# Kernel optimization log

Hardware: AMD Instinct MI355X
Metric: run time of the kernel (lower is better)

## Reference

```python
import jax, jax.numpy as jnp
import numpy as np

D_MODEL = 1024
NUM_HEADS = 16
D_K = D_MODEL // NUM_HEADS
BATCH = 2
SEQ = 2048


def setup_inputs() -> dict:
    key = jax.random.key(0)
    ks = jax.random.split(key, 11)
    s = 1.0 / np.sqrt(D_MODEL)
    return {
        "query": jax.random.normal(ks[0], (BATCH, SEQ, D_MODEL), jnp.float32),
        "key_": jax.random.normal(ks[1], (BATCH, SEQ, D_MODEL), jnp.float32),
        "value": jax.random.normal(ks[2], (BATCH, SEQ, D_MODEL), jnp.float32),
        "w_q": jax.random.uniform(ks[3], (D_MODEL, D_MODEL), jnp.float32, -s, s),
        "b_q": jax.random.uniform(ks[4], (D_MODEL,), jnp.float32, -s, s),
        "w_k": jax.random.uniform(ks[5], (D_MODEL, D_MODEL), jnp.float32, -s, s),
        "b_k": jax.random.uniform(ks[6], (D_MODEL,), jnp.float32, -s, s),
        "w_v": jax.random.uniform(ks[7], (D_MODEL, D_MODEL), jnp.float32, -s, s),
        "b_v": jax.random.uniform(ks[8], (D_MODEL,), jnp.float32, -s, s),
        "w_o": jax.random.uniform(ks[9], (D_MODEL, D_MODEL), jnp.float32, -s, s),
        "b_o": jax.random.uniform(ks[10], (D_MODEL,), jnp.float32, -s, s),
    }


def reference(query, key_, value, w_q, b_q, w_k, b_k, w_v, b_v, w_o, b_o):
    B, S, D = query.shape
    H, dk = NUM_HEADS, D_K

    def proj(x, w, b):
        # torch Linear: x @ w.T + b ; reshape to (B, H, S, dk)
        return (x @ w.T + b).reshape(B, S, H, dk).transpose(0, 2, 1, 3)

    Q = proj(query, w_q, b_q)
    K = proj(key_, w_k, b_k)
    V = proj(value, w_v, b_v)

    scores = jnp.einsum("bhqd,bhkd->bhqk", Q, K) / jnp.sqrt(jnp.float32(dk))
    attn = jax.nn.softmax(scores, axis=-1)  # dropout is identity in eval
    ctx = jnp.einsum("bhqk,bhkd->bhqd", attn, V)
    ctx = ctx.transpose(0, 2, 1, 3).reshape(B, S, D)
    out = ctx @ w_o.T + b_o
    return out
```

## Files before the change

### kernel.cpp

```cpp
#include <hip/hip_runtime.h>
#include <cstdint>
#include <cstddef>

typedef unsigned short u16;
typedef short bf16x8 __attribute__((ext_vector_type(8)));
typedef unsigned short u16x8 __attribute__((ext_vector_type(8)));
typedef float f32x4 __attribute__((ext_vector_type(4)));

#define NHEAD 16
#define SEQ 2048
#define DMODEL 1024
#define BATCH 2
#define QSCALE 0.18033688011112042f

__device__ __forceinline__ float exp2_fast(float x) {
  return __builtin_amdgcn_exp2f(x);
}

__device__ __forceinline__ u16 f2bf(float f) {
  union { float f; unsigned u; } v; v.f = f;
  return (u16)((v.u + 0x7fffu + ((v.u >> 16) & 1u)) >> 16);
}

__device__ __forceinline__ int swz(int row, int colbyte) {
  return (row << 7) + (colbyte ^ ((row & 7) << 4));
}

__device__ __forceinline__ void load_lds16(const void* g, void* lds) {
  __builtin_amdgcn_global_load_lds(
      (const __attribute__((address_space(1))) unsigned int*)g,
      (__attribute__((address_space(3))) unsigned int*)lds, 16, 0, 0);
}

__global__ __launch_bounds__(256) void convall(
    const float* __restrict__ q, const float* __restrict__ k, const float* __restrict__ v,
    const float* __restrict__ wq, const float* __restrict__ wk,
    const float* __restrict__ wv, const float* __restrict__ wo,
    u16* __restrict__ Xq, u16* __restrict__ Xk, u16* __restrict__ Xv,
    u16* __restrict__ Wq, u16* __restrict__ Wk, u16* __restrict__ Wv,
    u16* __restrict__ Wo) {
  int bid = blockIdx.x;
  const float* in;
  u16* out;
  int local;
  if (bid < 6144) {
    int a = bid >> 11;
    local = bid & 2047;
    in = a == 0 ? q : a == 1 ? k : v;
    out = a == 0 ? Xq : a == 1 ? Xk : Xv;
  } else {
    int bb = bid - 6144;
    int a = bb >> 9;
    local = bb & 511;
    in = a == 0 ? wq : a == 1 ? wk : a == 2 ? wv : wo;
    out = a == 0 ? Wq : a == 1 ? Wk : a == 2 ? Wv : Wo;
  }
  int i = local * 256 + threadIdx.x;
  const float4* p = (const float4*)in + (size_t)i * 2;
  float4 a4 = p[0], b4 = p[1];
  u16x8 o;
  o[0] = f2bf(a4.x); o[1] = f2bf(a4.y); o[2] = f2bf(a4.z); o[3] = f2bf(a4.w);
  o[4] = f2bf(b4.x); o[5] = f2bf(b4.y); o[6] = f2bf(b4.z); o[7] = f2bf(b4.w);
  *((u16x8*)out + i) = o;
}

__global__ __launch_bounds__(256) void gemm_qkv(
    const u16* __restrict__ A0, const u16* __restrict__ A1, const u16* __restrict__ A2,
    const u16* __restrict__ W0, const u16* __restrict__ W1, const u16* __restrict__ W2,
    const float* __restrict__ b0, const float* __restrict__ b1, const float* __restrict__ b2,
    u16* __restrict__ C0, u16* __restrict__ C1, u16* __restrict__ C2) {
  constexpr int K = 1024;
  __shared__ u16 Ash[128 * 32];
  __shared__ u16 Bsh[128 * 32];
  const int z = blockIdx.z;
  const u16* A = z == 0 ? A0 : z == 1 ? A1 : A2;
  const u16* W = z == 0 ? W0 : z == 1 ? W1 : W2;
  const float* bias = z == 0 ? b0 : z == 1 ? b1 : b2;
  u16* C = z == 0 ? C0 : z == 1 ? C1 : C2;
  const float scale = z == 0 ? QSCALE : 1.0f;

  const int t = threadIdx.x;
  const int w = t >> 6;
  const int l = t & 63;
  const int m0 = (blockIdx.x * 4 + (blockIdx.y >> 3)) * 128;
  const int n0 = (blockIdx.y & 7) * 128;
  const int wm = (w >> 1) * 64;
  const int wn = (w & 1) * 64;
  const int lr = l & 15;
  const int hi = l >> 4;
  const int lk = hi * 8;
  const int srow = l >> 2;
  const int scol = (l & 3) * 8;

  f32x4 acc[4][4] = {};

  for (int k0 = 0; k0 < K; k0 += 32) {
#pragma unroll
    for (int c = 0; c < 2; ++c) {
      int ra = (c * 4 + w) * 16 + srow;
      load_lds16(A + (size_t)(m0 + ra) * K + k0 + scol, &Ash[(c * 4 + w) * 512]);
      load_lds16(W + (size_t)(n0 + ra) * K + k0 + scol, &Bsh[(c * 4 + w) * 512]);
    }
    __syncthreads();
    bf16x8 af[4], bfr[4];
#pragma unroll
    for (int i = 0; i < 4; ++i)
      af[i] = *(const bf16x8*)&Ash[(wm + i * 16 + lr) * 32 + lk];
#pragma unroll
    for (int j = 0; j < 4; ++j)
      bfr[j] = *(const bf16x8*)&Bsh[(wn + j * 16 + lr) * 32 + lk];
#pragma unroll
    for (int i = 0; i < 4; ++i)
#pragma unroll
      for (int j = 0; j < 4; ++j)
        acc[i][j] = __builtin_amdgcn_mfma_f32_16x16x32_bf16(af[i], bfr[j], acc[i][j], 0, 0, 0);
    __syncthreads();
  }

#pragma unroll
  for (int i = 0; i < 4; ++i)
#pragma unroll
    for (int j = 0; j < 4; ++j)
#pragma unroll
      for (int r = 0; r < 4; ++r) {
        int row = m0 + wm + i * 16 + hi * 4 + r;
        int col = n0 + wn + j * 16 + lr;
        float v = (acc[i][j][r] + bias[col]) * scale;
        int b = row >> 11, s = row & 2047;
        int h = col >> 6, d = col & 63;
        C[(((size_t)(b * NHEAD + h) * SEQ + s) << 6) + d] = f2bf(v);
      }
}

__global__ __launch_bounds__(256) void gemm_o(const u16* __restrict__ A,
                                              const u16* __restrict__ W,
                                              const float* __restrict__ bias,
                                              float* __restrict__ C) {
  constexpr int K = 1024;
  __shared__ u16 Ash[64 * 32];
  __shared__ u16 Bsh[128 * 32];
  const int t = threadIdx.x;
  const int w = t >> 6;
  const int l = t & 63;
  const int m0 = (blockIdx.x * 8 + (blockIdx.y >> 3)) * 64;
  const int n0 = (blockIdx.y & 7) * 128;
  const int wm = (w >> 1) * 32;
  const int wn = (w & 1) * 64;
  const int lr = l & 15;
  const int hi = l >> 4;
  const int lk = hi * 8;
  const int srow = l >> 2;
  const int scol = (l & 3) * 8;

  f32x4 acc[2][4] = {};

  for (int k0 = 0; k0 < K; k0 += 32) {
    {
      int ra = w * 16 + srow;
      load_lds16(A + (size_t)(m0 + ra) * K + k0 + scol, &Ash[w * 512]);
    }
#pragma unroll
    for (int c = 0; c < 2; ++c) {
      int rb = (c * 4 + w) * 16 + srow;
      load_lds16(W + (size_t)(n0 + rb) * K + k0 + scol, &Bsh[(c * 4 + w) * 512]);
    }
    __syncthreads();
    bf16x8 af[2], bfr[4];
#pragma unroll
    for (int i = 0; i < 2; ++i)
      af[i] = *(const bf16x8*)&Ash[(wm + i * 16 + lr) * 32 + lk];
#pragma unroll
    for (int j = 0; j < 4; ++j)
      bfr[j] = *(const bf16x8*)&Bsh[(wn + j * 16 + lr) * 32 + lk];
#pragma unroll
    for (int i = 0; i < 2; ++i)
#pragma unroll
      for (int j = 0; j < 4; ++j)
        acc[i][j] = __builtin_amdgcn_mfma_f32_16x16x32_bf16(af[i], bfr[j], acc[i][j], 0, 0, 0);
    __syncthreads();
  }

#pragma unroll
  for (int i = 0; i < 2; ++i)
#pragma unroll
    for (int j = 0; j < 4; ++j)
#pragma unroll
      for (int r = 0; r < 4; ++r) {
        int row = m0 + wm + i * 16 + hi * 4 + r;
        int col = n0 + wn + j * 16 + lr;
        C[(size_t)row * DMODEL + col] = acc[i][j][r] + bias[col];
      }
}

__global__ __launch_bounds__(256) void transpose_v(const u16* __restrict__ V,
                                                   u16* __restrict__ Vt) {
  __shared__ u16 tile[64][72];
  int st = blockIdx.x, bh = blockIdx.y;
  int t = threadIdx.x;
  {
    int s = t >> 2, part = (t & 3) * 16;
    const u16* g = V + (((size_t)bh * SEQ + st * 64 + s) << 6) + part;
    u16x8 v0 = *(const u16x8*)&g[0];
    u16x8 v1 = *(const u16x8*)&g[8];
    *(u16x8*)&tile[s][part] = v0;
    *(u16x8*)&tile[s][part + 8] = v1;
  }
  __syncthreads();
  {
    int d = t >> 2, sp = (t & 3) * 16;
    u16x8 o0, o1;
#pragma unroll
    for (int j = 0; j < 8; ++j) {
      int c0 = sp + j, c1 = sp + 8 + j;
      o0[j] = tile[(c0 & 3) * 16 + (c0 >> 2)][d];
      o1[j] = tile[(c1 & 3) * 16 + (c1 >> 2)][d];
    }
    u16* out = Vt + ((size_t)bh * 64 + d) * SEQ + st * 64 + sp;
    *(u16x8*)&out[0] = o0;
    *(u16x8*)&out[8] = o1;
  }
}

__device__ __forceinline__ void attn_tile(
    int kt, bool pf, const u16* Kg, const u16* Vg, int srow, int scb,
    char* QsB, char* KsC, char* VsC, char* KsN, char* VsN,
    bf16x8 (&qf)[2][2], f32x4 (&acc)[2][4], float (&lsum)[2][4],
    int w, int lr, int hi) {
  u16x8 nk0, nk1, nv0, nv1;
  if (pf) {
    const u16* kg = Kg + (kt + 1) * 4096;
    const u16* vg = Vg + (kt + 1) * 64;
    nk0 = *(const u16x8*)&kg[srow * 64 + scb / 2];
    nk1 = *(const u16x8*)&kg[srow * 64 + scb / 2 + 8];
    nv0 = *(const u16x8*)&vg[(size_t)srow * SEQ + scb / 2];
    nv1 = *(const u16x8*)&vg[(size_t)srow * SEQ + scb / 2 + 8];
  }

  f32x4 sc[2][4] = {};
  __builtin_amdgcn_s_setprio(1);
#pragma unroll
  for (int ks = 0; ks < 2; ++ks) {
    bf16x8 kb[4];
#pragma unroll
    for (int nt = 0; nt < 4; ++nt)
      kb[nt] = *(const bf16x8*)(KsC + swz(nt * 16 + lr, ks * 64 + hi * 16));
#pragma unroll
    for (int mt = 0; mt < 2; ++mt)
#pragma unroll
      for (int nt = 0; nt < 4; ++nt)
        sc[mt][nt] = __builtin_amdgcn_mfma_f32_16x16x32_bf16(qf[mt][ks], kb[nt], sc[mt][nt], 0, 0, 0);
  }
  __builtin_amdgcn_s_setprio(0);

#pragma unroll
  for (int mt = 0; mt < 2; ++mt)
#pragma unroll
    for (int r = 0; r < 4; ++r) {
      int prow = w * 32 + mt * 16 + hi * 4 + r;
      float p0 = exp2_fast(sc[mt][0][r]);
      float p1 = exp2_fast(sc[mt][1][r]);
      float p2 = exp2_fast(sc[mt][2][r]);
      float p3 = exp2_fast(sc[mt][3][r]);
      lsum[mt][r] += (p0 + p1) + (p2 + p3);
      uint2 pk;
      asm("v_cvt_pk_bf16_f32 %0, %1, %2" : "=v"(pk.x) : "v"(p0), "v"(p1));
      asm("v_cvt_pk_bf16_f32 %0, %1, %2" : "=v"(pk.y) : "v"(p2), "v"(p3));
      *(uint2*)(QsB + swz(prow, lr * 8)) = pk;
    }

  asm volatile("" ::: "memory");

  __builtin_amdgcn_s_setprio(1);
#pragma unroll
  for (int ks = 0; ks < 2; ++ks) {
    bf16x8 pa[2], vb[4];
#pragma unroll
    for (int mt = 0; mt < 2; ++mt)
      pa[mt] = *(const bf16x8*)(QsB + swz(w * 32 + mt * 16 + lr, ks * 64 + hi * 16));
#pragma unroll
    for (int nt = 0; nt < 4; ++nt)
      vb[nt] = *(const bf16x8*)(VsC + swz(nt * 16 + lr, ks * 64 + hi * 16));
#pragma unroll
    for (int mt = 0; mt < 2; ++mt)
#pragma unroll
      for (int nt = 0; nt < 4; ++nt)
        acc[mt][nt] = __builtin_amdgcn_mfma_f32_16x16x32_bf16(pa[mt], vb[nt], acc[mt][nt], 0, 0, 0);
  }
  __builtin_amdgcn_s_setprio(0);

  if (pf) {
    *(u16x8*)(KsN + swz(srow, scb)) = nk0;
    *(u16x8*)(KsN + swz(srow, scb + 16)) = nk1;
    *(u16x8*)(VsN + swz(srow, scb)) = nv0;
    *(u16x8*)(VsN + swz(srow, scb + 16)) = nv1;
  }
  __syncthreads();
}

__global__ __launch_bounds__(256) void attn(const u16* __restrict__ Q,
                                            const u16* __restrict__ K,
                                            const u16* __restrict__ Vt,
                                            u16* __restrict__ ctx) {
  __shared__ u16 Qs[128 * 64];
  __shared__ u16 Ks[2][64 * 64];
  __shared__ u16 Vs[2][64 * 64];
  char* const QsB = (char*)Qs;

  const int t = threadIdx.x, w = t >> 6, l = t & 63;
  const int lr = l & 15, hi = l >> 4;

  const int bid = blockIdx.x;
  const int idx = bid >> 3;
  const int bh = (bid & 7) * 4 + (idx >> 4);
  const int q0 = (idx & 15) * 128;

  const u16* Qg = Q + ((size_t)bh * SEQ + q0) * 64;
  const u16* Kg = K + (size_t)bh * SEQ * 64;
  const u16* Vg = Vt + (size_t)bh * 64 * SEQ;

#pragma unroll
  for (int i = 0; i < 4; ++i) {
    int c = i * 256 + t;
    int row = c >> 3, cb = (c & 7) * 16;
    u16x8 qv = *(const u16x8*)&Qg[row * 64 + cb / 2];
    *(u16x8*)(QsB + swz(row, cb)) = qv;
  }
  const int srow = t >> 2;
  const int scb = (t & 3) * 32;
  {
    u16x8 k0 = *(const u16x8*)&Kg[srow * 64 + scb / 2];
    u16x8 k1 = *(const u16x8*)&Kg[srow * 64 + scb / 2 + 8];
    u16x8 v0 = *(const u16x8*)&Vg[(size_t)srow * SEQ + scb / 2];
    u16x8 v1 = *(const u16x8*)&Vg[(size_t)srow * SEQ + scb / 2 + 8];
    char* KsB = (char*)Ks[0];
    char* VsB = (char*)Vs[0];
    *(u16x8*)(KsB + swz(srow, scb)) = k0;
    *(u16x8*)(KsB + swz(srow, scb + 16)) = k1;
    *(u16x8*)(VsB + swz(srow, scb)) = v0;
    *(u16x8*)(VsB + swz(srow, scb + 16)) = v1;
  }
  __syncthreads();

  bf16x8 qf[2][2];
#pragma unroll
  for (int mt = 0; mt < 2; ++mt)
#pragma unroll
    for (int ks = 0; ks < 2; ++ks)
      qf[mt][ks] = *(const bf16x8*)(QsB + swz(w * 32 + mt * 16 + lr, ks * 64 + hi * 16));

  f32x4 acc[2][4] = {};
  float lsum[2][4] = {{0.f, 0.f, 0.f, 0.f}, {0.f, 0.f, 0.f, 0.f}};

  for (int kt2 = 0; kt2 < SEQ / 128; ++kt2) {
    attn_tile(2 * kt2, true, Kg, Vg, srow, scb, QsB,
              (char*)Ks[0], (char*)Vs[0], (char*)Ks[1], (char*)Vs[1],
              qf, acc, lsum, w, lr, hi);
    attn_tile(2 * kt2 + 1, kt2 < SEQ / 128 - 1, Kg, Vg, srow, scb, QsB,
              (char*)Ks[1], (char*)Vs[1], (char*)Ks[0], (char*)Vs[0],
              qf, acc, lsum, w, lr, hi);
  }

  const int b = bh >> 4, h = bh & 15;
#pragma unroll
  for (int mt = 0; mt < 2; ++mt)
#pragma unroll
    for (int r = 0; r < 4; ++r) {
      float s = lsum[mt][r];
      s += __shfl_xor(s, 1);
      s += __shfl_xor(s, 2);
      s += __shfl_xor(s, 4);
      s += __shfl_xor(s, 8);
      float inv = 1.0f / s;
      int srow_ = q0 + w * 32 + mt * 16 + hi * 4 + r;
#pragma unroll
      for (int nt = 0; nt < 4; ++nt) {
        int d = nt * 16 + lr;
        ctx[((size_t)(b * SEQ + srow_)) * DMODEL + h * 64 + d] =
            f2bf(acc[mt][nt][r] * inv);
      }
    }
}

extern "C" void kernel_launch(void* const* d_in, const int* in_sizes, int n_in,
                              void* d_out, int out_size, void* d_ws, size_t ws_size,
                              hipStream_t stream) {
  const float* q  = (const float*)d_in[0];
  const float* k  = (const float*)d_in[1];
  const float* v  = (const float*)d_in[2];
  const float* wq = (const float*)d_in[3];
  const float* bq = (const float*)d_in[4];
  const float* wk = (const float*)d_in[5];
  const float* bk = (const float*)d_in[6];
  const float* wv = (const float*)d_in[7];
  const float* bv = (const float*)d_in[8];
  const float* wo = (const float*)d_in[9];
  const float* bo = (const float*)d_in[10];

  const size_t XB = (size_t)4096 * 1024 * 2;
  const size_t WB = (size_t)1024 * 1024 * 2;
  char* ws = (char*)d_ws;
  u16* Xq = (u16*)(ws);
  u16* Xk = (u16*)(ws + XB);
  u16* Xv = (u16*)(ws + 2 * XB);
  u16* Wq = (u16*)(ws + 3 * XB);
  u16* Wk = (u16*)(ws + 3 * XB + WB);
  u16* Wv = (u16*)(ws + 3 * XB + 2 * WB);
  u16* Wo = (u16*)(ws + 3 * XB + 3 * WB);
  u16* Qb = (u16*)(ws + 4 * XB);
  u16* Kb = (u16*)(ws + 5 * XB);
  u16* Vb = (u16*)(ws + 6 * XB);
  u16* Vtb = Xk;
  u16* ctxb = Xq;

  convall<<<8192, 256, 0, stream>>>(q, k, v, wq, wk, wv, wo,
                                    Xq, Xk, Xv, Wq, Wk, Wv, Wo);

  gemm_qkv<<<dim3(8, 32, 3), 256, 0, stream>>>(Xq, Xk, Xv, Wq, Wk, Wv,
                                               bq, bk, bv, Qb, Kb, Vb);

  transpose_v<<<dim3(SEQ / 64, BATCH * NHEAD), 256, 0, stream>>>(Vb, Vtb);

  attn<<<512, 256, 0, stream>>>(Qb, Kb, Vtb, ctxb);

  gemm_o<<<dim3(8, 64), 256, 0, stream>>>(ctxb, Wo, bo, (float*)d_out);
}
```

Measured before the change: 124.2 us.

## Fuse fp32-to-bf16 activation conversion into QKV GEMM A-tile loads

Removes the separate conversion pass over the query/key/value activations. The QKV GEMM now reads fp32 activations directly, converts them to bf16 in registers and stores them to shared memory, while weights are still pre-converted by a smaller kernel. This avoids writing and re-reading three bf16 activation copies, but the GEMM reads twice the A bytes for each tile and swaps the async global-to-LDS load for synchronous register loads. Each activation tile is also re-converted by all eight column blocks.

```diff
diff --git a/kernel.cpp b/kernel.cpp
--- a/kernel.cpp
+++ b/kernel.cpp
@@ -22,6 +22,12 @@
   return (u16)((v.u + 0x7fffu + ((v.u >> 16) & 1u)) >> 16);
 }
 
+__device__ __forceinline__ unsigned cvt_pk(float a, float b) {
+  unsigned r;
+  asm("v_cvt_pk_bf16_f32 %0, %1, %2" : "=v"(r) : "v"(a), "v"(b));
+  return r;
+}
+
 __device__ __forceinline__ int swz(int row, int colbyte) {
   return (row << 7) + (colbyte ^ ((row & 7) << 4));
 }
@@ -32,29 +38,16 @@
       (__attribute__((address_space(3))) unsigned int*)lds, 16, 0, 0);
 }
 
-__global__ __launch_bounds__(256) void convall(
-    const float* __restrict__ q, const float* __restrict__ k, const float* __restrict__ v,
+__global__ __launch_bounds__(256) void wconv(
     const float* __restrict__ wq, const float* __restrict__ wk,
     const float* __restrict__ wv, const float* __restrict__ wo,
-    u16* __restrict__ Xq, u16* __restrict__ Xk, u16* __restrict__ Xv,
     u16* __restrict__ Wq, u16* __restrict__ Wk, u16* __restrict__ Wv,
     u16* __restrict__ Wo) {
   int bid = blockIdx.x;
-  const float* in;
-  u16* out;
-  int local;
-  if (bid < 6144) {
-    int a = bid >> 11;
-    local = bid & 2047;
-    in = a == 0 ? q : a == 1 ? k : v;
-    out = a == 0 ? Xq : a == 1 ? Xk : Xv;
-  } else {
-    int bb = bid - 6144;
-    int a = bb >> 9;
-    local = bb & 511;
-    in = a == 0 ? wq : a == 1 ? wk : a == 2 ? wv : wo;
-    out = a == 0 ? Wq : a == 1 ? Wk : a == 2 ? Wv : Wo;
-  }
+  int a = bid >> 9;
+  int local = bid & 511;
+  const float* in = a == 0 ? wq : a == 1 ? wk : a == 2 ? wv : wo;
+  u16* out = a == 0 ? Wq : a == 1 ? Wk : a == 2 ? Wv : Wo;
   int i = local * 256 + threadIdx.x;
   const float4* p = (const float4*)in + (size_t)i * 2;
   float4 a4 = p[0], b4 = p[1];
@@ -65,7 +58,7 @@
 }
 
 __global__ __launch_bounds__(256) void gemm_qkv(
-    const u16* __restrict__ A0, const u16* __restrict__ A1, const u16* __restrict__ A2,
+    const float* __restrict__ A0, const float* __restrict__ A1, const float* __restrict__ A2,
     const u16* __restrict__ W0, const u16* __restrict__ W1, const u16* __restrict__ W2,
     const float* __restrict__ b0, const float* __restrict__ b1, const float* __restrict__ b2,
     u16* __restrict__ C0, u16* __restrict__ C1, u16* __restrict__ C2) {
@@ -73,7 +66,7 @@
   __shared__ u16 Ash[128 * 32];
   __shared__ u16 Bsh[128 * 32];
   const int z = blockIdx.z;
-  const u16* A = z == 0 ? A0 : z == 1 ? A1 : A2;
+  const float* A = z == 0 ? A0 : z == 1 ? A1 : A2;
   const u16* W = z == 0 ? W0 : z == 1 ? W1 : W2;
   const float* bias = z == 0 ? b0 : z == 1 ? b1 : b2;
   u16* C = z == 0 ? C0 : z == 1 ? C1 : C2;
@@ -91,15 +84,30 @@
   const int lk = hi * 8;
   const int srow = l >> 2;
   const int scol = (l & 3) * 8;
+  const int ar = t >> 1;
+  const int ac = (t & 1) * 16;
 
   f32x4 acc[4][4] = {};
 
   for (int k0 = 0; k0 < K; k0 += 32) {
 #pragma unroll
     for (int c = 0; c < 2; ++c) {
-      int ra = (c * 4 + w) * 16 + srow;
-      load_lds16(A + (size_t)(m0 + ra) * K + k0 + scol, &Ash[(c * 4 + w) * 512]);
-      load_lds16(W + (size_t)(n0 + ra) * K + k0 + scol, &Bsh[(c * 4 + w) * 512]);
+      int rb = (c * 4 + w) * 16 + srow;
+      load_lds16(W + (size_t)(n0 + rb) * K + k0 + scol, &Bsh[(c * 4 + w) * 512]);
+    }
+    {
+      const float* Af = A + (size_t)(m0 + ar) * K + k0 + ac;
+      f32x4 f0 = *(const f32x4*)&Af[0];
+      f32x4 f1 = *(const f32x4*)&Af[4];
+      f32x4 f2 = *(const f32x4*)&Af[8];
+      f32x4 f3 = *(const f32x4*)&Af[12];
+      uint4 o;
+      o.x = cvt_pk(f0[0], f0[1]); o.y = cvt_pk(f0[2], f0[3]);
+      o.z = cvt_pk(f1[0], f1[1]); o.w = cvt_pk(f1[2], f1[3]);
+      *(uint4*)&Ash[ar * 32 + ac] = o;
+      o.x = cvt_pk(f2[0], f2[1]); o.y = cvt_pk(f2[2], f2[3]);
+      o.z = cvt_pk(f3[0], f3[1]); o.w = cvt_pk(f3[2], f3[3]);
+      *(uint4*)&Ash[ar * 32 + ac + 8] = o;
     }
     __syncthreads();
     bf16x8 af[4], bfr[4];
@@ -263,8 +271,8 @@
       float p3 = exp2_fast(sc[mt][3][r]);
       lsum[mt][r] += (p0 + p1) + (p2 + p3);
       uint2 pk;
-      asm("v_cvt_pk_bf16_f32 %0, %1, %2" : "=v"(pk.x) : "v"(p0), "v"(p1));
-      asm("v_cvt_pk_bf16_f32 %0, %1, %2" : "=v"(pk.y) : "v"(p2), "v"(p3));
+      pk.x = cvt_pk(p0, p1);
+      pk.y = cvt_pk(p2, p3);
       *(uint2*)(QsB + swz(prow, lr * 8)) = pk;
     }
 
@@ -399,9 +407,8 @@
   const size_t XB = (size_t)4096 * 1024 * 2;
   const size_t WB = (size_t)1024 * 1024 * 2;
   char* ws = (char*)d_ws;
-  u16* Xq = (u16*)(ws);
-  u16* Xk = (u16*)(ws + XB);
-  u16* Xv = (u16*)(ws + 2 * XB);
+  u16* ctxb = (u16*)(ws);
+  u16* Vtb = (u16*)(ws + XB);
   u16* Wq = (u16*)(ws + 3 * XB);
   u16* Wk = (u16*)(ws + 3 * XB + WB);
   u16* Wv = (u16*)(ws + 3 * XB + 2 * WB);
@@ -409,13 +416,10 @@
   u16* Qb = (u16*)(ws + 4 * XB);
   u16* Kb = (u16*)(ws + 5 * XB);
   u16* Vb = (u16*)(ws + 6 * XB);
-  u16* Vtb = Xk;
-  u16* ctxb = Xq;
-
-  convall<<<8192, 256, 0, stream>>>(q, k, v, wq, wk, wv, wo,
-                                    Xq, Xk, Xv, Wq, Wk, Wv, Wo);
-
-  gemm_qkv<<<dim3(8, 32, 3), 256, 0, stream>>>(Xq, Xk, Xv, Wq, Wk, Wv,
+
+  wconv<<<2048, 256, 0, stream>>>(wq, wk, wv, wo, Wq, Wk, Wv, Wo);
+
+  gemm_qkv<<<dim3(8, 32, 3), 256, 0, stream>>>(q, k, v, Wq, Wk, Wv,
                                                bq, bk, bv, Qb, Kb, Vb);
 
   transpose_v<<<dim3(SEQ / 64, BATCH * NHEAD), 256, 0, stream>>>(Vb, Vtb);
```

Measured after the change: 125.8 us. About the same (+1.4%).
